# Performance work log

Measured on AMD Instinct MI355X. Metric: run time of the kernel, lower is better.

## Reference

```python
import jax, jax.numpy as jnp
import numpy as np

MAX_DISP = 10
KS = 2 * MAX_DISP + 1  # 21 -> 441 displacements


def setup_inputs() -> dict:
    key = jax.random.key(0)
    k1, k2 = jax.random.split(key)
    B, C, H, W = 4, 64, 128, 128
    feat1 = jax.random.normal(k1, (B, C, H, W), dtype=jnp.float32)
    feat2 = jax.random.normal(k2, (B, C, H, W), dtype=jnp.float32)
    return {"feat1": feat1, "feat2": feat2}


def _correlation(feat1, feat2):
    B, C, H, W = feat1.shape
    pad = MAX_DISP
    feat2_p = jnp.pad(feat2, ((0, 0), (0, 0), (pad, pad), (pad, pad)))

    # all (i, j) displacements, flattened row-major to match torch cat order
    ii, jj = jnp.meshgrid(jnp.arange(KS), jnp.arange(KS), indexing="ij")
    shifts = jnp.stack([ii.ravel(), jj.ravel()], axis=-1)  # [KS*KS, 2]

    def one_shift(ij):
        i, j = ij[0], ij[1]
        f2 = jax.lax.dynamic_slice(feat2_p, (0, 0, i, j), (B, C, H, W))
        # reduce over channel dim only; avoid materializing product per-shift
        return jnp.einsum("bchw,bchw->bhw", feat1, f2) / C

    corr = jax.vmap(one_shift)(shifts)            # [KS*KS, B, H, W]
    return jnp.transpose(corr, (1, 0, 2, 3))      # [B, KS*KS, H, W]


def reference(feat1, feat2):
    return _correlation(feat1, feat2)
```

## Files before the change

### kernel.cpp

```cpp
#include <hip/hip_runtime.h>

#define BB  4
#define CC  64
#define HH  128
#define WW  128
#define KS  21
#define PAD 10
#define HWs (HH*WW)
#define LROW 160
#define LBUF (8*LROW)

typedef float f32x4n __attribute__((ext_vector_type(4)));

__global__ __launch_bounds__(256, 3) void corr_kernel(
    const float* __restrict__ feat1,
    const float* __restrict__ feat2,
    float* __restrict__ out)
{
    __shared__ __align__(16) float lds[2*LBUF];

    const int tid = threadIdx.x;
    int bi = blockIdx.x;
    const int di = bi % KS;  bi /= KS;
    const int h8 = bi % (HH/8);
    const int b  = bi / (HH/8);

    const int row = tid >> 5;
    const int q   = tid & 31;
    const int h   = h8*8 + row;
    const int w0  = q << 2;
    const int rr  = h + di - PAD;
    const bool valid = (rr >= 0) && (rr < HH);

    {
        const int L = (q < 12) ? q : (q + 128);
        lds[row*LROW + L]        = 0.0f;
        lds[LBUF + row*LROW + L] = 0.0f;
    }

    float acc[4][KS];
#pragma unroll
    for (int p = 0; p < 4; ++p)
#pragma unroll
        for (int d = 0; d < KS; ++d) acc[p][d] = 0.0f;

    if (__ballot(valid) != 0ull) {
        const float* f1p = feat1 + (((ptrdiff_t)b*CC*HH + h)*WW + w0);
        const float* f2p = feat2 + (((ptrdiff_t)b*CC*HH + rr)*WW + w0);

        float*       lw = &lds[row*LROW + 12 + w0];
        const float* lr = &lds[row*LROW + w0];

        const bool in0 = valid && (w0 >= 12);
        const bool in1 = valid && (w0 >= 8);

        float4 vcur = make_float4(0.f,0.f,0.f,0.f);
        float4 vnxt = make_float4(0.f,0.f,0.f,0.f);
        float2 g0   = make_float2(0.f,0.f);
        float4 g1   = make_float4(0.f,0.f,0.f,0.f);
        if (valid) {
            vcur = *(const float4*)(f2p);
            vnxt = *(const float4*)(f2p + HWs);
        }
        if (in0) g0 = *(const float2*)(f2p - 10);
        if (in1) g1 = *(const float4*)(f2p - 8);
        float4 a = *(const float4*)(f1p);

        *(float4*)lw = vcur;
        __builtin_amdgcn_sched_barrier(0);

#pragma unroll 2
        for (int c = 0; c < CC; ++c) {
            float4 an  = a;
            float2 g0n = make_float2(0.f,0.f);
            float4 g1n = make_float4(0.f,0.f,0.f,0.f);
            float4 vld = make_float4(0.f,0.f,0.f,0.f);
            if (c + 1 < CC) {
                an = *(const float4*)(f1p + HWs);
                if (in0) g0n = *(const float2*)(f2p + HWs - 10);
                if (in1) g1n = *(const float4*)(f2p + HWs - 8);
                if (valid && (c + 2 < CC)) vld = *(const float4*)(f2p + 2*HWs);
            }

            const float* lrb = lr + ((c & 1) ? LBUF : 0);
            const float4 w08 = *(const float4*)(lrb + 8);
            const float4 w16 = *(const float4*)(lrb + 16);
            const float4 w20 = *(const float4*)(lrb + 20);
            const float2 w24 = *(const float2*)(lrb + 24);

            *(float4*)(lw + ((c & 1) ? 0 : LBUF)) = vnxt;
            __builtin_amdgcn_sched_barrier(0);

            float win[28];
            win[2]=g0.x;   win[3]=g0.y;
            win[4]=g1.x;   win[5]=g1.y;   win[6]=g1.z;   win[7]=g1.w;
            win[8]=w08.x;  win[9]=w08.y;  win[10]=w08.z; win[11]=w08.w;
            win[12]=vcur.x; win[13]=vcur.y; win[14]=vcur.z; win[15]=vcur.w;
            win[16]=w16.x; win[17]=w16.y; win[18]=w16.z; win[19]=w16.w;
            win[20]=w20.x; win[21]=w20.y; win[22]=w20.z; win[23]=w20.w;
            win[24]=w24.x; win[25]=w24.y;

#pragma unroll
            for (int d = 0; d < KS; ++d) {
                acc[0][d] += a.x * win[d + 2];
                acc[1][d] += a.y * win[d + 3];
                acc[2][d] += a.z * win[d + 4];
                acc[3][d] += a.w * win[d + 5];
            }

            a = an; g0 = g0n; g1 = g1n; vcur = vnxt; vnxt = vld;
            f1p += HWs; f2p += HWs;
        }
    }

    const float scale = 1.0f / (float)CC;
    float* op = out + ((((ptrdiff_t)b*(KS*KS) + di*KS)*HH + h)*WW + w0);
#pragma unroll
    for (int d = 0; d < KS; ++d) {
        f32x4n v = { acc[0][d]*scale, acc[1][d]*scale,
                     acc[2][d]*scale, acc[3][d]*scale };
        __builtin_nontemporal_store(v, (f32x4n*)(op + (ptrdiff_t)d*HWs));
    }
}

extern "C" void kernel_launch(void* const* d_in, const int* in_sizes, int n_in,
                              void* d_out, int out_size, void* d_ws, size_t ws_size,
                              hipStream_t stream) {
    const float* feat1 = (const float*)d_in[0];
    const float* feat2 = (const float*)d_in[1];
    float* out = (float*)d_out;

    const int blocks = BB * (HH / 8) * KS;
    corr_kernel<<<blocks, 256, 0, stream>>>(feat1, feat2, out);
}
```

Baseline: 211.0 us.

## Split horizontal displacements across two thread groups and remap blocks across XCDs

Each block now has 512 threads in two groups of 256. Each group computes 11 of the 21 horizontal displacements, with one overlapping displacement whose store group 1 skips. Each group keeps its own double-buffered LDS rows, and the global halo loads are dropped in favour of zero-padded LDS reads. The block index is also permuted so that consecutive hardware blocks spread across the 8 XCDs. This halves accumulator registers per thread to allow higher occupancy and more parallelism, at the cost of redundant feat1/feat2 loads per group and a small amount of duplicated FMA work.

```diff
diff --git a/kernel.cpp b/kernel.cpp
--- a/kernel.cpp
+++ b/kernel.cpp
@@ -12,58 +12,56 @@
 
 typedef float f32x4n __attribute__((ext_vector_type(4)));
 
-__global__ __launch_bounds__(256, 3) void corr_kernel(
+__global__ __launch_bounds__(512, 4) void corr_kernel(
     const float* __restrict__ feat1,
     const float* __restrict__ feat2,
     float* __restrict__ out)
 {
-    __shared__ __align__(16) float lds[2*LBUF];
+    __shared__ __align__(16) float lds[4*LBUF];
 
     const int tid = threadIdx.x;
-    int bi = blockIdx.x;
+    const int g   = tid >> 8;
+    const int t   = tid & 255;
+
+    const int nwg = BB * (HH/8) * KS;
+    int bi = (blockIdx.x & 7) * (nwg >> 3) + (blockIdx.x >> 3);
+
     const int di = bi % KS;  bi /= KS;
     const int h8 = bi % (HH/8);
     const int b  = bi / (HH/8);
 
-    const int row = tid >> 5;
-    const int q   = tid & 31;
+    const int row = t >> 5;
+    const int q   = t & 31;
     const int h   = h8*8 + row;
     const int w0  = q << 2;
     const int rr  = h + di - PAD;
     const bool valid = (rr >= 0) && (rr < HH);
+    const int rc  = valid ? rr : 0;
 
-    {
-        const int L = (q < 12) ? q : (q + 128);
-        lds[row*LROW + L]        = 0.0f;
-        lds[LBUF + row*LROW + L] = 0.0f;
-    }
+    float* gb = &lds[(g*2)*LBUF];
+    { const int L = (q < 12) ? q : (q + 128);
+      gb[row*LROW + L]        = 0.0f;
+      gb[LBUF + row*LROW + L] = 0.0f; }
 
-    float acc[4][KS];
+    float acc[4][11];
 #pragma unroll
     for (int p = 0; p < 4; ++p)
 #pragma unroll
-        for (int d = 0; d < KS; ++d) acc[p][d] = 0.0f;
+        for (int j = 0; j < 11; ++j) acc[p][j] = 0.0f;
 
     if (__ballot(valid) != 0ull) {
-        const float* f1p = feat1 + (((ptrdiff_t)b*CC*HH + h)*WW + w0);
-        const float* f2p = feat2 + (((ptrdiff_t)b*CC*HH + rr)*WW + w0);
+        const float* f1p = feat1 + (((ptrdiff_t)(b*CC)*HH + h)*WW + w0);
+        const float* f2p = feat2 + (((ptrdiff_t)(b*CC)*HH + rc)*WW + w0);
 
-        float*       lw = &lds[row*LROW + 12 + w0];
-        const float* lr = &lds[row*LROW + w0];
-
-        const bool in0 = valid && (w0 >= 12);
-        const bool in1 = valid && (w0 >= 8);
+        float*       lw = gb + row*LROW + 12 + w0;
+        const float* lr = gb + row*LROW + w0;
 
         float4 vcur = make_float4(0.f,0.f,0.f,0.f);
         float4 vnxt = make_float4(0.f,0.f,0.f,0.f);
-        float2 g0   = make_float2(0.f,0.f);
-        float4 g1   = make_float4(0.f,0.f,0.f,0.f);
         if (valid) {
             vcur = *(const float4*)(f2p);
             vnxt = *(const float4*)(f2p + HWs);
         }
-        if (in0) g0 = *(const float2*)(f2p - 10);
-        if (in1) g1 = *(const float4*)(f2p - 8);
         float4 a = *(const float4*)(f1p);
 
         *(float4*)lw = vcur;
@@ -72,54 +70,55 @@
 #pragma unroll 2
         for (int c = 0; c < CC; ++c) {
             float4 an  = a;
-            float2 g0n = make_float2(0.f,0.f);
-            float4 g1n = make_float4(0.f,0.f,0.f,0.f);
             float4 vld = make_float4(0.f,0.f,0.f,0.f);
-            if (c + 1 < CC) {
-                an = *(const float4*)(f1p + HWs);
-                if (in0) g0n = *(const float2*)(f2p + HWs - 10);
-                if (in1) g1n = *(const float4*)(f2p + HWs - 8);
-                if (valid && (c + 2 < CC)) vld = *(const float4*)(f2p + 2*HWs);
-            }
+            if (c + 1 < CC) an = *(const float4*)(f1p + HWs);
+            if (valid && (c + 2 < CC)) vld = *(const float4*)(f2p + 2*HWs);
 
             const float* lrb = lr + ((c & 1) ? LBUF : 0);
-            const float4 w08 = *(const float4*)(lrb + 8);
-            const float4 w16 = *(const float4*)(lrb + 16);
-            const float4 w20 = *(const float4*)(lrb + 20);
-            const float2 w24 = *(const float2*)(lrb + 24);
+            float win[14];
+            if (g == 0) {
+                const float2 wl = *(const float2*)(lrb + 2);
+                const float4 wa = *(const float4*)(lrb + 4);
+                const float4 wb = *(const float4*)(lrb + 8);
+                win[0]=wl.x;  win[1]=wl.y;
+                win[2]=wa.x;  win[3]=wa.y;  win[4]=wa.z;  win[5]=wa.w;
+                win[6]=wb.x;  win[7]=wb.y;  win[8]=wb.z;  win[9]=wb.w;
+                win[10]=vcur.x; win[11]=vcur.y; win[12]=vcur.z; win[13]=vcur.w;
+            } else {
+                const float4 wa = *(const float4*)(lrb + 16);
+                const float4 wb = *(const float4*)(lrb + 20);
+                const float2 wl = *(const float2*)(lrb + 24);
+                win[0]=vcur.x; win[1]=vcur.y; win[2]=vcur.z; win[3]=vcur.w;
+                win[4]=wa.x;  win[5]=wa.y;  win[6]=wa.z;  win[7]=wa.w;
+                win[8]=wb.x;  win[9]=wb.y;  win[10]=wb.z; win[11]=wb.w;
+                win[12]=wl.x; win[13]=wl.y;
+            }
 
             *(float4*)(lw + ((c & 1) ? 0 : LBUF)) = vnxt;
             __builtin_amdgcn_sched_barrier(0);
 
-            float win[28];
-            win[2]=g0.x;   win[3]=g0.y;
-            win[4]=g1.x;   win[5]=g1.y;   win[6]=g1.z;   win[7]=g1.w;
-            win[8]=w08.x;  win[9]=w08.y;  win[10]=w08.z; win[11]=w08.w;
-            win[12]=vcur.x; win[13]=vcur.y; win[14]=vcur.z; win[15]=vcur.w;
-            win[16]=w16.x; win[17]=w16.y; win[18]=w16.z; win[19]=w16.w;
-            win[20]=w20.x; win[21]=w20.y; win[22]=w20.z; win[23]=w20.w;
-            win[24]=w24.x; win[25]=w24.y;
-
 #pragma unroll
-            for (int d = 0; d < KS; ++d) {
-                acc[0][d] += a.x * win[d + 2];
-                acc[1][d] += a.y * win[d + 3];
-                acc[2][d] += a.z * win[d + 4];
-                acc[3][d] += a.w * win[d + 5];
+            for (int j = 0; j < 11; ++j) {
+                acc[0][j] += a.x * win[j + 0];
+                acc[1][j] += a.y * win[j + 1];
+                acc[2][j] += a.z * win[j + 2];
+                acc[3][j] += a.w * win[j + 3];
             }
 
-            a = an; g0 = g0n; g1 = g1n; vcur = vnxt; vnxt = vld;
+            a = an; vcur = vnxt; vnxt = vld;
             f1p += HWs; f2p += HWs;
         }
     }
 
     const float scale = 1.0f / (float)CC;
-    float* op = out + ((((ptrdiff_t)b*(KS*KS) + di*KS)*HH + h)*WW + w0);
+    const int djb = 10 * g;
+    float* op = out + ((((ptrdiff_t)b*(KS*KS) + (ptrdiff_t)(di*KS + djb))*HH + h)*WW + w0);
 #pragma unroll
-    for (int d = 0; d < KS; ++d) {
-        f32x4n v = { acc[0][d]*scale, acc[1][d]*scale,
-                     acc[2][d]*scale, acc[3][d]*scale };
-        __builtin_nontemporal_store(v, (f32x4n*)(op + (ptrdiff_t)d*HWs));
+    for (int j = 0; j < 11; ++j) {
+        if (g == 1 && j == 0) continue;
+        f32x4n v = { acc[0][j]*scale, acc[1][j]*scale,
+                     acc[2][j]*scale, acc[3][j]*scale };
+        __builtin_nontemporal_store(v, (f32x4n*)(op + (ptrdiff_t)j*HWs));
     }
 }
 
@@ -131,5 +130,5 @@
     float* out = (float*)d_out;
 
     const int blocks = BB * (HH / 8) * KS;
-    corr_kernel<<<blocks, 256, 0, stream>>>(feat1, feat2, out);
+    corr_kernel<<<blocks, 512, 0, stream>>>(feat1, feat2, out);
 }
```

Result: slower. 264.8 us (+25.5%).
